# Kernel tuning notes

Hardware: AMD Instinct MI355X
Metric: run time of the kernel (lower is better)

## Reference

```python
import jax, jax.numpy as jnp
import numpy as np

NUM_REC = 22
P = 24            # nodes per graph
G = 8192          # graphs in batch
N = G * P         # 196608 nodes
E = N * 4         # 786432 edges (avg degree 4)
F_NODE = 96       # 74 chem features + 22 receptor one-hot
F_EDGE = 16
EPS = 1e-5
NEG_SLOPE = 0.2   # GATv2 default negative_slope


def gatv2(x, src, dst, edge_attr, Wl, bl, Wr, br, We, att, bo):
    """PyG GATv2Conv (heads=1, add_self_loops=True, fill_value='mean'), eval mode."""
    n = x.shape[0]
    # self loops with edge_attr = mean of incoming edge attrs per target node
    deg = jax.ops.segment_sum(jnp.ones_like(dst, dtype=x.dtype), dst, num_segments=n)
    loop_attr = jax.ops.segment_sum(edge_attr, dst, num_segments=n) / jnp.maximum(deg, 1.0)[:, None]
    loop = jnp.arange(n, dtype=src.dtype)
    s = jnp.concatenate([src, loop])           # [E+N] source
    d = jnp.concatenate([dst, loop])           # [E+N] target
    ea = jnp.concatenate([edge_attr, loop_attr], axis=0)
    xl = x @ Wl + bl                           # source transform [n, C]
    xr = x @ Wr + br                           # target transform [n, C]
    m = xl[s] + xr[d] + ea @ We                # [E+N, C]
    e = jax.nn.leaky_relu(m, NEG_SLOPE) @ att  # [E+N] attention logits
    # segment softmax over target nodes (every node has its self loop -> no empty segment)
    emax = jax.ops.segment_max(e, d, num_segments=n)
    ez = jnp.exp(e - emax[d])
    denom = jax.ops.segment_sum(ez, d, num_segments=n)
    alpha = ez / denom[d]
    return jax.ops.segment_sum(alpha[:, None] * xl[s], d, num_segments=n) + bo


def batchnorm(h, gamma, beta):
    # training-style BN (batch statistics, biased var) as in torch BatchNorm1d forward
    mu = h.mean(0)
    var = h.var(0)
    return gamma * (h - mu) * jax.lax.rsqrt(var + EPS) + beta


def setup_inputs() -> dict:
    key = jax.random.key(0)
    ks = jax.random.split(key, 40)
    x = jax.random.normal(ks[0], (N, F_NODE), jnp.float32)
    # intra-graph, self-loop-free edges
    src = jax.random.randint(ks[1], (E,), 0, N)
    off = jax.random.randint(ks[2], (E,), 1, P)
    dst = (src // P) * P + (src % P + off) % P
    edge_index = jnp.stack([src, dst]).astype(jnp.int32)
    edge_attr = jax.random.normal(ks[3], (E, F_EDGE), jnp.float32)
    batch = (jnp.arange(N) // P).astype(jnp.int32)

    def lin(k, i, o):
        return jax.random.normal(k, (i, o), jnp.float32) * 0.1

    def vec(k, o):
        return jax.random.normal(k, (o,), jnp.float32) * 0.1

    Fin = F_NODE - NUM_REC  # 74
    return {
        "x": x, "edge_index": edge_index, "edge_attr": edge_attr, "batch": batch,
        # GATv2 layer 1 (74 -> 32)
        "Wl1": lin(ks[4], Fin, 32), "bl1": vec(ks[5], 32),
        "Wr1": lin(ks[6], Fin, 32), "br1": vec(ks[7], 32),
        "We1": lin(ks[8], F_EDGE, 32), "att1": vec(ks[9], 32), "bo1": vec(ks[10], 32),
        # GATv2 layer 2 (32 -> 8)
        "Wl2": lin(ks[11], 32, 8), "bl2": vec(ks[12], 8),
        "Wr2": lin(ks[13], 32, 8), "br2": vec(ks[14], 8),
        "We2": lin(ks[15], F_EDGE, 8), "att2": vec(ks[16], 8), "bo2": vec(ks[17], 8),
        # BatchNorm affine
        "g1": jnp.ones((32,), jnp.float32), "be1": jnp.zeros((32,), jnp.float32),
        "g2": jnp.ones((8,), jnp.float32), "be2": jnp.zeros((8,), jnp.float32),
        # MLP head (8+22=30 -> 32 -> 16 -> 8 -> 4 -> 2)
        "fc1_W": lin(ks[18], 8 + NUM_REC, 32), "fc1_b": vec(ks[19], 32),
        "fc2_W": lin(ks[20], 32, 16), "fc2_b": vec(ks[21], 16),
        "fc3_W": lin(ks[22], 16, 8), "fc3_b": vec(ks[23], 8),
        "fc4_W": lin(ks[24], 8, 4), "fc4_b": vec(ks[25], 4),
        "out_W": lin(ks[26], 4, 2), "out_b": vec(ks[27], 2),
    }


def reference(x, edge_index, edge_attr, batch,
              Wl1, bl1, Wr1, br1, We1, att1, bo1,
              Wl2, bl2, Wr2, br2, We2, att2, bo2,
              g1, be1, g2, be2,
              fc1_W, fc1_b, fc2_W, fc2_b, fc3_W, fc3_b, fc4_W, fc4_b, out_W, out_b):
    src, dst = edge_index[0], edge_index[1]
    # per-graph receptor features = last NUM_REC cols of the first node of each graph
    first_idx = jnp.searchsorted(batch, jnp.arange(G, dtype=batch.dtype))
    rec_feat = x[first_idx, -NUM_REC:]                       # [G, 22]
    xin = x[:, :-NUM_REC]                                    # [N, 74]

    h = jax.nn.relu(gatv2(xin, src, dst, edge_attr, Wl1, bl1, Wr1, br1, We1, att1, bo1))
    h = batchnorm(h, g1, be1)                                # [N, 32]
    h = jax.nn.sigmoid(gatv2(h, src, dst, edge_attr, Wl2, bl2, Wr2, br2, We2, att2, bo2))
    h = batchnorm(h, g2, be2)                                # [N, 8]

    cnt = jax.ops.segment_sum(jnp.ones((x.shape[0], 1), x.dtype), batch, num_segments=G)
    pooled = jax.ops.segment_sum(h, batch, num_segments=G) / cnt  # global_mean_pool [G, 8]

    z = jnp.concatenate([pooled, rec_feat], axis=1)          # [G, 30]
    z = jax.nn.relu(z @ fc1_W + fc1_b)
    z = jax.nn.relu(z @ fc2_W + fc2_b)
    z = jax.nn.relu(z @ fc3_W + fc3_b)
    z = jax.nn.relu(z @ fc4_W + fc4_b)
    return z @ out_W + out_b                                 # [G, 2]
```

## Files before the change

kernel.cpp:

```cpp
#include <hip/hip_runtime.h>

typedef unsigned short u16;
typedef unsigned int   u32;
typedef __attribute__((ext_vector_type(4))) float f4_t;
typedef __attribute__((ext_vector_type(4))) unsigned short us4_t;

#define GG 8192
#define PP 24
#define NN 196608
#define EE 786432
#define CAP 176

#define oWl1 0
#define oWr1 2368
#define obl1 4736
#define obr1 4768
#define oWe1 4800
#define oatt1 5312
#define obo1 5344
#define oWl2 5376
#define oWr2 5632
#define obl2 5888
#define obr2 5896
#define oWe2 5904
#define oatt2 6032
#define obo2 6040
#define ofc1W 6048
#define ofc1b 7008
#define ofc2W 7040
#define ofc2b 7552
#define ofc3W 7568
#define ofc3b 7696
#define ofc4W 7704
#define ofc4b 7736
#define ooutW 7740
#define ooutb 7748

#define oW1I 0
#define oW2P 4864
#define oB2P 5376

__device__ __forceinline__ float bf2f(u16 u){
  union { u32 i; float f; } x; x.i = ((u32)u) << 16; return x.f;
}
__device__ __forceinline__ u32 fkey(float f){
  int i = __float_as_int(f);
  return (i >= 0) ? (((u32)i) | 0x80000000u) : ~((u32)i);
}
__device__ __forceinline__ float funkey(u32 k){
  u32 i = (k & 0x80000000u) ? (k & 0x7FFFFFFFu) : ~k;
  return __uint_as_float(i);
}
__device__ __forceinline__ float lrelu(float m){ return m > 0.f ? m : 0.2f*m; }
__device__ __forceinline__ float sexp(float a){ return __expf(fminf(a, 0.f)); }
__device__ __forceinline__ float ldf(const void* p, size_t i, int isf){
  return isf ? ((const float*)p)[i] : bf2f(((const u16*)p)[i]);
}

__global__ void k_zero(float* __restrict__ out){
  int i = blockIdx.x*256 + threadIdx.x;
  if(i < GG*2) out[i] = 0.f;
}

__global__ void k_count(const int* __restrict__ dst, int* __restrict__ cnt){
  int e = blockIdx.x*256 + threadIdx.x;
  if(e < EE){
    u32 d = (u32)dst[e];
    if(d < (u32)NN) atomicAdd(&cnt[d], 1);
  }
}

__global__ void k_scanA(const int* __restrict__ cnt, int* __restrict__ offs,
                        int* __restrict__ bsum){
  __shared__ int part[1024];
  int t = threadIdx.x;
  int i = blockIdx.x*1024 + t;
  int c = cnt[i];
  part[t] = c; __syncthreads();
  for(int off=1; off<1024; off<<=1){
    int v = (t>=off) ? part[t-off] : 0;
    __syncthreads();
    part[t] += v;
    __syncthreads();
  }
  offs[i] = part[t] - c;
  if(t==1023) bsum[blockIdx.x] = part[1023];
}

__global__ void k_scanB(int* __restrict__ bsum, int* __restrict__ offs){
  __shared__ int part[256];
  int t = threadIdx.x;
  int c = (t < 192) ? bsum[t] : 0;
  part[t] = c; __syncthreads();
  for(int off=1; off<256; off<<=1){
    int v = (t>=off) ? part[t-off] : 0;
    __syncthreads();
    part[t] += v;
    __syncthreads();
  }
  if(t < 192) bsum[t] = part[t] - c;
  if(t == 255) offs[NN] = part[255];
}

__global__ void k_scanC(int* __restrict__ offs, const int* __restrict__ bsum,
                        int* __restrict__ cursor){
  int t = threadIdx.x;
  int i = blockIdx.x*1024 + t;
  int v = offs[i] + bsum[blockIdx.x];
  offs[i] = v;
  cursor[i] = v;
}

__global__ void k_scatter(const int* __restrict__ src, const int* __restrict__ dst,
                          int* __restrict__ cursor, int* __restrict__ spack){
  int e = blockIdx.x*256 + threadIdx.x;
  if(e < EE){
    u32 d = (u32)dst[e];
    if(d >= (u32)NN) return;
    int g = d / PP;
    int pos = atomicAdd(&cursor[d], 1);
    if((u32)pos < (u32)EE){
      int sl = src[e] - g*PP;
      if((u32)sl > 23u) sl = 0;
      spack[pos] = sl | ((int)(d - g*PP) << 5) | (e << 10);
    }
  }
}

__global__ void k_eaperm(const int* __restrict__ spack, const int* __restrict__ offs,
                         const void* __restrict__ ea, const int* __restrict__ dflag,
                         float* __restrict__ eap){
  int i = blockIdx.x*256 + threadIdx.x;
  if(i >= EE) return;
  if(i >= offs[NN]) return;
  int isf = dflag[0];
  u32 id = ((u32)spack[i]) >> 10;
  if(id >= (u32)EE) id = 0;
  float* o = eap + (size_t)i*16;
  if(isf){
    const float* er = (const float*)ea + (size_t)id*16;
    #pragma unroll
    for(int q=0;q<4;q++) *(f4_t*)(o + q*4) = *(const f4_t*)(er + q*4);
  } else {
    const u16* er = (const u16*)ea + (size_t)id*16;
    #pragma unroll
    for(int c=0;c<16;c++) o[c] = bf2f(er[c]);
  }
}

__global__ void k_eapermB(const int* __restrict__ spack, const int* __restrict__ offs,
                          const void* __restrict__ ea, const int* __restrict__ dflag,
                          const float* __restrict__ wb,
                          float* __restrict__ eap, float* __restrict__ p2){
  int i = blockIdx.x*256 + threadIdx.x;
  if(i >= EE) return;
  if(i >= offs[NN]) return;
  int isf = dflag[0];
  u32 id = ((u32)spack[i]) >> 10;
  if(id >= (u32)EE) id = 0;
  float eav[16];
  if(isf){
    const float* er = (const float*)ea + (size_t)id*16;
    #pragma unroll
    for(int k=0;k<16;k++) eav[k] = er[k];
  } else {
    const u16* er = (const u16*)ea + (size_t)id*16;
    #pragma unroll
    for(int k=0;k<16;k++) eav[k] = bf2f(er[k]);
  }
  float* o = eap + (size_t)i*16;
  #pragma unroll
  for(int q=0;q<4;q++){
    f4_t r; r[0]=eav[q*4+0]; r[1]=eav[q*4+1]; r[2]=eav[q*4+2]; r[3]=eav[q*4+3];
    *(f4_t*)(o + q*4) = r;
  }
  float* o2 = p2 + (size_t)i*8;
  #pragma unroll
  for(int c=0;c<8;c+=4){
    float s0=0.f, s1=0.f, s2=0.f, s3=0.f;
    #pragma unroll
    for(int k=0;k<16;k++){
      f4_t w = *(const f4_t*)(wb + oWe2 + k*8 + c);
      s0 += eav[k]*w[0]; s1 += eav[k]*w[1]; s2 += eav[k]*w[2]; s3 += eav[k]*w[3];
    }
    f4_t r; r[0]=s0; r[1]=s1; r[2]=s2; r[3]=s3;
    *(f4_t*)(o2 + c) = r;
  }
}

__global__ void k_wconv(float* __restrict__ wb, float* __restrict__ wq, int* __restrict__ dflag,
    const u32* __restrict__ xw,
    const void* Wl1, const void* bl1, const void* Wr1, const void* br1,
    const void* We1, const void* att1, const void* bo1,
    const void* Wl2, const void* bl2, const void* Wr2, const void* br2,
    const void* We2, const void* att2, const void* bo2,
    const void* f1W, const void* f1b, const void* f2W, const void* f2b,
    const void* f3W, const void* f3b, const void* f4W, const void* f4b,
    const void* oW,  const void* ob)
{
  __shared__ u32 mx[256];
  int t = threadIdx.x;
  u32 m = 0;
  for(int i=t; i<2048; i+=256){
    u32 e = (xw[i] >> 7) & 0xFFu;
    m = m > e ? m : e;
  }
  mx[t] = m; __syncthreads();
  for(int off=128; off>0; off>>=1){
    if(t<off) mx[t] = mx[t] > mx[t+off] ? mx[t] : mx[t+off];
    __syncthreads();
  }
  int isf = (mx[0] > 140u) ? 1 : 0;
  if(t==0) dflag[0] = isf;
  #define CP(off,src,len) for(int i=t;i<(len);i+=256) wb[(off)+i]=ldf(src,i,isf);
  CP(oWl1,Wl1,2368) CP(oWr1,Wr1,2368) CP(obl1,bl1,32) CP(obr1,br1,32)
  CP(oWe1,We1,512)  CP(oatt1,att1,32) CP(obo1,bo1,32)
  CP(oWl2,Wl2,256)  CP(oWr2,Wr2,256)  CP(obl2,bl2,8)  CP(obr2,br2,8)
  CP(oWe2,We2,128)  CP(oatt2,att2,8)  CP(obo2,bo2,8)
  CP(ofc1W,f1W,960) CP(ofc1b,f1b,32)  CP(ofc2W,f2W,512) CP(ofc2b,f2b,16)
  CP(ofc3W,f3W,128) CP(ofc3b,f3b,8)   CP(ofc4W,f4W,32)  CP(ofc4b,f4b,4)
  CP(ooutW,oW,8)    CP(ooutb,ob,2)
  #undef CP
  for(int i=t; i<76*64; i+=256){
    int k = i>>6, cc = i&63, mat = cc>>5, c = cc&31;
    wq[oW1I + i] = (k < 74) ? ldf(mat ? Wr1 : Wl1, k*32 + c, isf) : 0.f;
  }
}

__global__ void k_prep2(float* __restrict__ wq, const float* __restrict__ wb,
                        const float* __restrict__ stats1){
  int t = threadIdx.x;
  for(int i=t; i<512; i+=256){
    int k = i>>4, cc = i&15, mat = cc>>3, c = cc&7;
    wq[oW2P + i] = stats1[k] * wb[(mat ? oWr2 : oWl2) + k*8 + c];
  }
  if(t < 16){
    int mat = t>>3, c = t&7;
    float s = wb[(mat ? obr2 : obl2) + c];
    for(int k=0;k<32;k++) s += stats1[32+k] * wb[(mat ? oWr2 : oWl2) + k*8 + c];
    wq[oB2P + t] = s;
  }
}

__global__ __launch_bounds__(256, 4) void k_l1stats_p(
    const void* __restrict__ x, const float* __restrict__ eap,
    const float* __restrict__ wb, const float* __restrict__ wq,
    const int* __restrict__ offs, const int* __restrict__ spack, const int* __restrict__ dflag,
    float* __restrict__ p1sum, float* __restrict__ p1sq,
    float* __restrict__ h1)
{
  __shared__ __align__(16) float sP[CAP][36];
  __shared__ __align__(16) float sXl[24][36];
  __shared__ __align__(16) float sXr[24][36];
  __shared__ __align__(16) float sPS[24][32];
  __shared__ __align__(16) float sPQ[24][32];
  __shared__ float sEv[CAP];
  __shared__ int   sSl[CAP];
  __shared__ int   sRO[25];

  const int t = threadIdx.x;
  const int g = blockIdx.x;
  const int isf = dflag[0];
  const int nb = g*PP;
  const int eb = offs[nb];
  int ecnt = offs[nb+24] - eb;
  if(ecnt < 0) ecnt = 0; if(ecnt > CAP) ecnt = CAP;

  if(t < 25){
    int v = offs[nb+t] - eb;
    if(v < 0) v = 0; if(v > CAP) v = CAP;
    sRO[t] = v;
  }
  for(int i=t; i<ecnt; i+=256){
    int sl = spack[eb+i] & 31; if(sl > 23) sl = 0;
    sSl[i] = sl;
  }

  {
    const int c = t & 31, mat = (t>>5)&1, w = t>>6, cc = t&63;
    const float* gW = wq + oW1I;
    float bi = wb[(mat ? obr1 : obl1) + c];
    float acc[6];
    #pragma unroll
    for(int j=0;j<6;j++) acc[j] = bi;
    if(isf){
      const float* xr0 = (const float*)x + (size_t)(nb + w*6)*96;
      for(int kb=0; kb<19; kb++){
        float w0 = gW[(kb*4+0)*64 + cc];
        float w1 = gW[(kb*4+1)*64 + cc];
        float w2 = gW[(kb*4+2)*64 + cc];
        float w3 = gW[(kb*4+3)*64 + cc];
        #pragma unroll
        for(int j=0;j<6;j++){
          f4_t xv = *(const f4_t*)(xr0 + (size_t)j*96 + kb*4);
          acc[j] += xv[0]*w0 + xv[1]*w1 + xv[2]*w2 + xv[3]*w3;
        }
      }
    } else {
      const u16* xr0 = (const u16*)x + (size_t)(nb + w*6)*96;
      for(int kb=0; kb<19; kb++){
        float w0 = gW[(kb*4+0)*64 + cc];
        float w1 = gW[(kb*4+1)*64 + cc];
        float w2 = gW[(kb*4+2)*64 + cc];
        float w3 = gW[(kb*4+3)*64 + cc];
        #pragma unroll
        for(int j=0;j<6;j++){
          us4_t xv = *(const us4_t*)(xr0 + (size_t)j*96 + kb*4);
          acc[j] += bf2f(xv[0])*w0 + bf2f(xv[1])*w1 + bf2f(xv[2])*w2 + bf2f(xv[3])*w3;
        }
      }
    }
    if(mat){
      #pragma unroll
      for(int j=0;j<6;j++) sXr[w*6+j][c] = acc[j];
    } else {
      #pragma unroll
      for(int j=0;j<6;j++) sXl[w*6+j][c] = acc[j];
    }
  }

  for(int i=t; i<ecnt*8; i+=256){
    int e = i>>3, q = i&7;
    const float* er = eap + (size_t)(eb+e)*16;
    float s0=0.f, s1=0.f, s2=0.f, s3=0.f;
    #pragma unroll
    for(int k=0;k<16;k++){
      float ev = er[k];
      f4_t w = *(const f4_t*)(wb + oWe1 + k*32 + q*4);
      s0 += ev*w[0]; s1 += ev*w[1]; s2 += ev*w[2]; s3 += ev*w[3];
    }
    f4_t r; r[0]=s0; r[1]=s1; r[2]=s2; r[3]=s3;
    *(f4_t*)&sP[e][q*4] = r;
  }
  __syncthreads();

  if(t < 192){
    const int r = t >> 3, sub = t & 7;
    const int a = sRO[r], b = sRO[r+1];
    const int deg = b - a;
    const float* att = wb + oatt1;

    float emax = -3.4e38f;
    for(int e=a+sub; e<b; e+=8){
      int sl = sSl[e];
      float ev = 0.f;
      #pragma unroll
      for(int q=0;q<8;q++){
        f4_t pv  = *(const f4_t*)&sP[e][q*4];
        f4_t xlv = *(const f4_t*)&sXl[sl][q*4];
        f4_t xrv = *(const f4_t*)&sXr[r][q*4];
        ev += att[q*4+0]*lrelu(xlv[0]+xrv[0]+pv[0]);
        ev += att[q*4+1]*lrelu(xlv[1]+xrv[1]+pv[1]);
        ev += att[q*4+2]*lrelu(xlv[2]+xrv[2]+pv[2]);
        ev += att[q*4+3]*lrelu(xlv[3]+xrv[3]+pv[3]);
      }
      sEv[e] = ev;
      emax = fmaxf(emax, ev);
    }
    emax = fmaxf(emax, __shfl_xor(emax, 1));
    emax = fmaxf(emax, __shfl_xor(emax, 2));
    emax = fmaxf(emax, __shfl_xor(emax, 4));

    float m0=0.f, m1=0.f, m2=0.f, m3=0.f;
    for(int e=a; e<b; ++e){
      f4_t pv = *(const f4_t*)&sP[e][sub*4];
      m0 += pv[0]; m1 += pv[1]; m2 += pv[2]; m3 += pv[3];
    }
    float invd = 1.f / (float)(deg > 0 ? deg : 1);
    float sv;
    {
      int c0 = sub*4;
      sv  = att[c0+0]*lrelu(sXl[r][c0+0] + sXr[r][c0+0] + m0*invd);
      sv += att[c0+1]*lrelu(sXl[r][c0+1] + sXr[r][c0+1] + m1*invd);
      sv += att[c0+2]*lrelu(sXl[r][c0+2] + sXr[r][c0+2] + m2*invd);
      sv += att[c0+3]*lrelu(sXl[r][c0+3] + sXr[r][c0+3] + m3*invd);
    }
    sv += __shfl_xor(sv, 1);
    sv += __shfl_xor(sv, 2);
    sv += __shfl_xor(sv, 4);

    float m = fmaxf(emax, sv);
    float ssum = 0.f;
    for(int e=a+sub; e<b; e+=8){
      float z = sexp(sEv[e] - m);
      sEv[e] = z;
      ssum += z;
    }
    ssum += __shfl_xor(ssum, 1);
    ssum += __shfl_xor(ssum, 2);
    ssum += __shfl_xor(ssum, 4);
    float selfZ = sexp(sv - m);
    float rden = 1.f / fmaxf(ssum + selfZ, 1e-30f);

    float a0=0.f, a1=0.f, a2=0.f, a3=0.f;
    for(int e=a; e<b; ++e){
      float z = sEv[e];
      f4_t xlv = *(const f4_t*)&sXl[sSl[e]][sub*4];
      a0 += z*xlv[0]; a1 += z*xlv[1]; a2 += z*xlv[2]; a3 += z*xlv[3];
    }
    f4_t xself = *(const f4_t*)&sXl[r][sub*4];
    f4_t outv, sqv;
    {
      float o;
      o = (a0 + selfZ*xself[0]) * rden; o = fmaxf(o + wb[obo1+sub*4+0], 0.f); outv[0]=o; sqv[0]=o*o;
      o = (a1 + selfZ*xself[1]) * rden; o = fmaxf(o + wb[obo1+sub*4+1], 0.f); outv[1]=o; sqv[1]=o*o;
      o = (a2 + selfZ*xself[2]) * rden; o = fmaxf(o + wb[obo1+sub*4+2], 0.f); outv[2]=o; sqv[2]=o*o;
      o = (a3 + selfZ*xself[3]) * rden; o = fmaxf(o + wb[obo1+sub*4+3], 0.f); outv[3]=o; sqv[3]=o*o;
    }
    *(f4_t*)&h1[((size_t)nb + r)*32 + sub*4] = outv;
    *(f4_t*)&sPS[r][sub*4] = outv;
    *(f4_t*)&sPQ[r][sub*4] = sqv;
  }
  __syncthreads();
  if(t < 32){
    float s=0.f, q=0.f;
    #pragma unroll
    for(int r=0;r<24;r++){ s += sPS[r][t]; q += sPQ[r][t]; }
    p1sum[g*32+t] = s; p1sq[g*32+t] = q;
  }
}

__global__ __launch_bounds__(256, 6) void k_fused2_p(
    const float* __restrict__ p2,
    const float* __restrict__ wb, const float* __restrict__ wq,
    const float* __restrict__ h1,
    const int* __restrict__ offs, const int* __restrict__ spack,
    float* __restrict__ gsum2, float* __restrict__ gsq2)
{
  __shared__ float sXl2[24][13];
  __shared__ float sXr2[24][13];
  __shared__ float sEv[CAP];
  __shared__ int   sSl[CAP];
  __shared__ int   sRO[25];
  __shared__ float sGS[24][8];
  __shared__ float sGQ[24][8];

  const int t = threadIdx.x;
  const int g = blockIdx.x;
  const int wid = t >> 6;
  const int lane = t & 63;
  const int nb = g*PP;
  const int eb = offs[nb];
  int ecnt = offs[nb+24] - eb;
  if(ecnt < 0) ecnt = 0; if(ecnt > CAP) ecnt = CAP;

  if(t < 25){
    int v = offs[nb+t] - eb;
    if(v < 0) v = 0; if(v > CAP) v = CAP;
    sRO[t] = v;
  }
  for(int i=t; i<ecnt; i+=256){
    int sl = spack[eb+i] & 31; if(sl > 23) sl = 0;
    sSl[i] = sl;
  }
  {
    int rz = wid*6;
    for(int i=lane; i<96; i+=64){
      int rl = i>>4, cc = i&15;
      int r = rz + rl;
      float s = wq[oB2P + cc];
      const float* hr = h1 + ((size_t)nb + r)*32;
      #pragma unroll
      for(int q=0;q<8;q++){
        f4_t hv = *(const f4_t*)(hr + q*4);
        s += hv[0]*wq[oW2P+(q*4+0)*16+cc] + hv[1]*wq[oW2P+(q*4+1)*16+cc]
           + hv[2]*wq[oW2P+(q*4+2)*16+cc] + hv[3]*wq[oW2P+(q*4+3)*16+cc];
      }
      if(cc < 8) sXl2[r][cc] = s; else sXr2[r][cc-8] = s;
    }
  }
  __syncthreads();

  if(t < 192){
    const int r = t >> 3, sub = t & 7;
    const int a = sRO[r], b = sRO[r+1];
    const int deg = b - a;
    const float* att2 = wb + oatt2;

    float emax = -3.4e38f;
    for(int e=a+sub; e<b; e+=8){
      int sl = sSl[e];
      const float* pe = p2 + (size_t)(eb+e)*8;
      float ev = 0.f;
      #pragma unroll
      for(int j=0;j<8;j++)
        ev += att2[j]*lrelu(sXl2[sl][j] + sXr2[r][j] + pe[j]);
      sEv[e] = ev;
      emax = fmaxf(emax, ev);
    }
    emax = fmaxf(emax, __shfl_xor(emax, 1));
    emax = fmaxf(emax, __shfl_xor(emax, 2));
    emax = fmaxf(emax, __shfl_xor(emax, 4));

    float mpc = 0.f;
    for(int e=a; e<b; ++e)
      mpc += p2[(size_t)(eb+e)*8 + sub];
    float invd = 1.f / (float)(deg > 0 ? deg : 1);
    float sv = att2[sub]*lrelu(sXl2[r][sub] + sXr2[r][sub] + mpc*invd);
    sv += __shfl_xor(sv, 1);
    sv += __shfl_xor(sv, 2);
    sv += __shfl_xor(sv, 4);

    float m = fmaxf(emax, sv);
    float ssum = 0.f;
    for(int e=a+sub; e<b; e+=8){
      float z = sexp(sEv[e] - m);
      sEv[e] = z;
      ssum += z;
    }
    ssum += __shfl_xor(ssum, 1);
    ssum += __shfl_xor(ssum, 2);
    ssum += __shfl_xor(ssum, 4);
    float selfZ = sexp(sv - m);
    float rden = 1.f / fmaxf(ssum + selfZ, 1e-30f);

    float acc = 0.f;
    for(int e=a; e<b; ++e)
      acc += sEv[e] * sXl2[sSl[e]][sub];
    float o = (acc + selfZ*sXl2[r][sub]) * rden;
    float s = 1.f / (1.f + __expf(-(o + wb[obo2+sub])));
    sGS[r][sub] = s;
    sGQ[r][sub] = s*s;
  }
  __syncthreads();
  if(t < 8){
    float gs=0.f, gq=0.f;
    #pragma unroll
    for(int r=0;r<24;r++){ gs += sGS[r][t]; gq += sGQ[r][t]; }
    gsum2[g*8+t] = gs; gsq2[g*8+t] = gq;
  }
}

__global__ __launch_bounds__(256, 6) void k_l1stats(
    const void* __restrict__ x, const void* __restrict__ ea, const float* __restrict__ eap,
    const float* __restrict__ wb, const float* __restrict__ wq,
    const int* __restrict__ offs, const int* __restrict__ spack, const int* __restrict__ dflag,
    float* __restrict__ p1sum, float* __restrict__ p1sq,
    float* __restrict__ h1, int use_h1)
{
  __shared__ __align__(16) float sEaF[CAP][16];
  __shared__ __align__(16) float sXl[24][36];
  __shared__ float sXr[24][33];
  __shared__ float sEaSum[24][17];
  __shared__ float sEv[CAP];
  __shared__ int   sSl[CAP];
  __shared__ int   sRO[25];
  __shared__ float sSelfE[24];
  __shared__ float sPS[4][32], sPQ[4][32];

  const int t = threadIdx.x;
  const int g = blockIdx.x;
  const int wid = t >> 6;
  const int lane = t & 63;
  const int isf = dflag[0];
  const int nb = g*PP;
  const int eb = offs[nb];
  int ecnt = offs[nb+24] - eb; if(ecnt < 0) ecnt = 0; if(ecnt > CAP) ecnt = CAP;

  if(t < 25){
    int v = offs[nb+t] - eb;
    if(v < 0) v = 0; if(v > CAP) v = CAP;
    sRO[t] = v;
  }
  if(eap){
    for(int i=t; i<ecnt; i+=256) sSl[i] = spack[eb+i] & 1023;
    for(int i=t; i<ecnt*4; i+=256){
      int e = i>>2, q = i&3;
      *(f4_t*)&sEaF[e][q*4] = *(const f4_t*)(eap + ((size_t)(eb+e))*16 + q*4);
    }
  } else {
    for(int i=t; i<ecnt; i+=256){
      int sp = spack[eb+i];
      sSl[i] = sp & 1023;
      u32 id = ((u32)sp) >> 10;
      if(id >= (u32)EE) id = 0;
      if(isf){
        const float* er = (const float*)ea + (size_t)id*16;
        #pragma unroll
        for(int q=0;q<4;q++) *(f4_t*)&sEaF[i][q*4] = *(const f4_t*)(er + q*4);
      } else {
        #pragma unroll
        for(int c=0;c<16;c++) sEaF[i][c] = bf2f(((const u16*)ea)[(size_t)id*16 + c]);
      }
    }
  }
  {
    int rz = wid*6;
    for(int i=lane; i<6*17; i+=64) sEaSum[rz + i/17][i%17] = 0.f;
  }

  {
    const int c = t & 31, mat = (t>>5)&1, w = wid, cc = t&63;
    const float* gW = wq + oW1I;
    float bi = wb[(mat ? obr1 : obl1) + c];
    float acc[6];
    #pragma unroll
    for(int j=0;j<6;j++) acc[j] = bi;
    if(isf){
      const float* xr0 = (const float*)x + (size_t)(nb + w*6)*96;
      for(int kb=0; kb<19; kb++){
        float w0 = gW[(kb*4+0)*64 + cc];
        float w1 = gW[(kb*4+1)*64 + cc];
        float w2 = gW[(kb*4+2)*64 + cc];
        float w3 = gW[(kb*4+3)*64 + cc];
        #pragma unroll
        for(int j=0;j<6;j++){
          f4_t xv = *(const f4_t*)(xr0 + (size_t)j*96 + kb*4);
          acc[j] += xv[0]*w0 + xv[1]*w1 + xv[2]*w2 + xv[3]*w3;
        }
      }
    } else {
      const u16* xr0 = (const u16*)x + (size_t)(nb + w*6)*96;
      for(int kb=0; kb<19; kb++){
        float w0 = gW[(kb*4+0)*64 + cc];
        float w1 = gW[(kb*4+1)*64 + cc];
        float w2 = gW[(kb*4+2)*64 + cc];
        float w3 = gW[(kb*4+3)*64 + cc];
        #pragma unroll
        for(int j=0;j<6;j++){
          us4_t xv = *(const us4_t*)(xr0 + (size_t)j*96 + kb*4);
          acc[j] += bf2f(xv[0])*w0 + bf2f(xv[1])*w1 + bf2f(xv[2])*w2 + bf2f(xv[3])*w3;
        }
      }
    }
    if(mat){
      #pragma unroll
      for(int j=0;j<6;j++) sXr[w*6+j][c] = acc[j];
    } else {
      #pragma unroll
      for(int j=0;j<6;j++) sXl[w*6+j][c] = acc[j];
    }
  }
  __syncthreads();

  const int r0 = wid*6;
  const int a0 = sRO[r0], a1 = sRO[r0+6];
  const int c = t & 31, eo = (t>>5)&1;

  float wr[16];
  #pragma unroll
  for(int k=0;k<16;k++) wr[k] = wb[oWe1 + k*32 + c];
  const float av = wb[oatt1 + c];
  const float bv = wb[obo1 + c];

  for(int base=a0; base<a1; base+=2){
    int e = base + eo;
    bool valid = (e < a1);
    int ec = valid ? e : a0;
    int sp = sSl[ec];
    int sl = sp & 31; if(sl > 23) sl = 0;
    int dl = (sp >> 5) & 31; if(dl > 23) dl = 0;
    f4_t A0 = *(const f4_t*)&sEaF[ec][0];
    f4_t A1 = *(const f4_t*)&sEaF[ec][4];
    f4_t A2 = *(const f4_t*)&sEaF[ec][8];
    f4_t A3 = *(const f4_t*)&sEaF[ec][12];
    float p = A0[0]*wr[0]+A0[1]*wr[1]+A0[2]*wr[2]+A0[3]*wr[3]
            + A1[0]*wr[4]+A1[1]*wr[5]+A1[2]*wr[6]+A1[3]*wr[7]
            + A2[0]*wr[8]+A2[1]*wr[9]+A2[2]*wr[10]+A2[3]*wr[11]
            + A3[0]*wr[12]+A3[1]*wr[13]+A3[2]*wr[14]+A3[3]*wr[15];
    if(valid && c < 16) atomicAdd(&sEaSum[dl][c], sEaF[ec][c]);
    float v = lrelu(sXl[sl][c] + sXr[dl][c] + p) * av;
    v += __shfl_xor(v, 16);
    v += __shfl_xor(v, 8);
    v += __shfl_xor(v, 4);
    v += __shfl_xor(v, 2);
    v += __shfl_xor(v, 1);
    if(valid && c == 0) sEv[e] = v;
  }

  #pragma unroll
  for(int rp=0; rp<3; rp++){
    int r = r0 + rp*2 + eo;
    int deg = sRO[r+1] - sRO[r];
    float invd = 1.f / (float)(deg > 0 ? deg : 1);
    float mp = 0.f;
    #pragma unroll
    for(int k=0;k<16;k++) mp += sEaSum[r][k] * wr[k];
    float v = lrelu(sXl[r][c] + sXr[r][c] + mp*invd) * av;
    v += __shfl_xor(v, 16);
    v += __shfl_xor(v, 8);
    v += __shfl_xor(v, 4);
    v += __shfl_xor(v, 2);
    v += __shfl_xor(v, 1);
    if(c == 0) sSelfE[r] = v;
  }

  float ps = 0.f, pq = 0.f;
  const int h = (t >> 5) & 1;
  #pragma unroll
  for(int j=0;j<6;j++){
    int r = r0 + j;
    int a = sRO[r], b = sRO[r+1];
    float selfE = sSelfE[r];
    float mx = -3.4e38f;
    for(int e=a+lane; e<b; e+=64) mx = fmaxf(mx, sEv[e]);
    mx = fmaxf(mx, __shfl_xor(mx, 32));
    mx = fmaxf(mx, __shfl_xor(mx, 16));
    mx = fmaxf(mx, __shfl_xor(mx, 8));
    mx = fmaxf(mx, __shfl_xor(mx, 4));
    mx = fmaxf(mx, __shfl_xor(mx, 2));
    mx = fmaxf(mx, __shfl_xor(mx, 1));
    float m = fmaxf(mx, selfE);
    float ds = 0.f;
    for(int e=a+lane; e<b; e+=64){
      float z = sexp(sEv[e] - m);
      sEv[e] = z;
      ds += z;
    }
    ds += __shfl_xor(ds, 32);
    ds += __shfl_xor(ds, 16);
    ds += __shfl_xor(ds, 8);
    ds += __shfl_xor(ds, 4);
    ds += __shfl_xor(ds, 2);
    ds += __shfl_xor(ds, 1);
// ... 193 lines not shown
    ds += __shfl_xor(ds, 8);
    ds += __shfl_xor(ds, 4);
    ds += __shfl_xor(ds, 2);
    ds += __shfl_xor(ds, 1);
    float selfZ = sexp(selfE - m);
    float rden = 1.f / fmaxf(ds + selfZ, 1e-30f);
    float acc = 0.f;
    for(int e=a+eo; e<b; e+=8){
      int sl = sSl[e] & 31; if(sl > 23) sl = 0;
      acc += sEv[e] * sXl2[sl][c];
    }
    acc += __shfl_xor(acc, 8);
    acc += __shfl_xor(acc, 16);
    acc += __shfl_xor(acc, 32);
    float out = (acc + selfZ * sXl2[r][c]) * rden;
    float s = 1.f / (1.f + __expf(-(out + bv)));
    if(eo == 0){ gs += s; gq += s*s; }
  }
  if(eo == 0){ sGS[wid][c] = gs; sGQ[wid][c] = gq; }
  __syncthreads();
  if(t < 8){
    gsum2[g*8+t] = sGS[0][t]+sGS[1][t]+sGS[2][t]+sGS[3][t];
    gsq2[g*8+t]  = sGQ[0][t]+sGQ[1][t]+sGQ[2][t]+sGQ[3][t];
  }
}

__global__ __launch_bounds__(256) void k_fused2_rec(
    const void* __restrict__ x, const void* __restrict__ ea,
    const float* __restrict__ wb, const float* __restrict__ stats1,
    const int* __restrict__ offs, const int* __restrict__ spack, const int* __restrict__ dflag,
    float* __restrict__ gsum2, float* __restrict__ gsq2)
{
  __shared__ float sXrow[24][76];
  __shared__ float sEaF[CAP][17];
  __shared__ __align__(16) float sXl[24][36];
  __shared__ __align__(16) float sXr[24][36];
  __shared__ __align__(16) float sOut[24][36];
  __shared__ float sH[24][33];
  __shared__ float sXl2[24][12], sXr2[24][12], sOut2[24][12];
  __shared__ float sEapSum[24][32];
  __shared__ float sEv[CAP], sEz[CAP];
  __shared__ int   sSp[CAP];
  __shared__ int   sDeg[24];
  __shared__ u32   sMaxU[24];
  __shared__ float sMaxF[24], sDen[24], sSelfZ[24];
  __shared__ float sAtt[32], sBo[32], sSc[32], sSh[32];

  const int t = threadIdx.x;
  const int g = blockIdx.x;
  const int isf = dflag[0];
  int eb = offs[g*24], ee = offs[(g+1)*24];
  if(eb < 0) eb = 0; if(eb > EE) eb = EE;
  if(ee < eb) ee = eb; if(ee > EE) ee = EE;
  int ecnt = ee - eb; if(ecnt > CAP) ecnt = CAP;

  for(int i=t; i<24*74; i+=256){
    int r = i/74, c = i%74;
    sXrow[r][c] = ldf(x, (size_t)(g*PP + r)*96 + c, isf);
  }
  for(int i=t; i<CAP; i+=256) sSp[i] = (i<ecnt) ? spack[eb+i] : 0;
  if(t < 32){ sAtt[t]=wb[oatt1+t]; sBo[t]=wb[obo1+t]; sSc[t]=stats1[t]; sSh[t]=stats1[32+t]; }
  if(t < 24){ sDeg[t]=0; sMaxU[t]=0u; sDen[t]=0.f; }
  for(int i=t; i<24*32; i+=256) sEapSum[i>>5][i&31] = 0.f;
  __syncthreads();
  for(int i=t; i<CAP*16; i+=256){
    int e = i>>4, c = i&15;
    float v = 0.f;
    if(e < ecnt){
      u32 id = ((u32)sSp[e]) >> 10;
      if(id >= (u32)EE) id = 0;
      v = ldf(ea, (size_t)id*16 + c, isf);
    }
    sEaF[e][c] = v;
  }
  __syncthreads();

  {
    int c = t & 31, rr0 = t >> 5;
    for(int r = rr0; r < 24; r += 8){
      float al = wb[obl1+c], ar = wb[obr1+c];
      for(int k=0;k<74;k++){
        float xv = sXrow[r][k];
        al += xv * wb[oWl1 + k*32 + c];
        ar += xv * wb[oWr1 + k*32 + c];
      }
      sXl[r][c] = al; sXr[r][c] = ar;
    }
  }
  __syncthreads();

  for(int e=t; e<ecnt; e+=256){
    int sp = sSp[e];
    int sl = sp & 31; if(sl > 23) sl = 0;
    int dl = (sp >> 5) & 31; if(dl > 23) dl = 0;
    float ev = 0.f;
    for(int c=0;c<32;c++){
      float p = 0.f;
      for(int k=0;k<16;k++) p += sEaF[e][k] * wb[oWe1 + k*32 + c];
      atomicAdd(&sEapSum[dl][c], p);
      ev += lrelu(sXl[sl][c] + sXr[dl][c] + p) * sAtt[c];
    }
    sEv[e] = ev;
    atomicMax(&sMaxU[dl], fkey(ev));
    atomicAdd(&sDeg[dl], 1);
  }
  __syncthreads();

  if(t < 24){
    float invd = 1.f / (float)(sDeg[t] > 0 ? sDeg[t] : 1);
    float ev = 0.f;
    for(int c=0;c<32;c++)
      ev += lrelu(sXl[t][c] + sXr[t][c] + sEapSum[t][c]*invd) * sAtt[c];
    float mxv = (sDeg[t] > 0) ? fmaxf(funkey(sMaxU[t]), ev) : ev;
    sMaxF[t] = mxv;
    float z = sexp(ev - mxv);
    sSelfZ[t] = z;
    sDen[t] = z;
  }
  __syncthreads();

  for(int e=t; e<ecnt; e+=256){
    int dl = (sSp[e]>>5)&31; if(dl > 23) dl = 0;
    float z = sexp(sEv[e] - sMaxF[dl]);
    sEz[e] = z;
    atomicAdd(&sDen[dl], z);
  }
  __syncthreads();

  for(int e=t; e<ecnt; e+=256){
    int dl = (sSp[e]>>5)&31; if(dl > 23) dl = 0;
    sEz[e] /= fmaxf(sDen[dl], 1e-30f);
  }
  if(t < 24) sSelfZ[t] /= fmaxf(sDen[t], 1e-30f);
  __syncthreads();

  for(int o=t; o<24*8; o+=256){
    int nl = o >> 3, cq = (o & 7)*4;
    float al = sSelfZ[nl];
    f4_t xv = *(const f4_t*)&sXl[nl][cq];
    f4_t r;
    #pragma unroll
    for(int j=0;j<4;j++) r[j] = al*xv[j];
    *(f4_t*)&sOut[nl][cq] = r;
  }
  __syncthreads();

  for(int o=t; o<ecnt*8; o+=256){
    int e = o >> 3, cq = (o & 7)*4;
    int sp = sSp[e];
    int sl = sp & 31; if(sl > 23) sl = 0;
    int dl = (sp >> 5) & 31; if(dl > 23) dl = 0;
    float al = sEz[e];
    f4_t xv = *(const f4_t*)&sXl[sl][cq];
    atomicAdd(&sOut[dl][cq+0], al*xv[0]);
    atomicAdd(&sOut[dl][cq+1], al*xv[1]);
    atomicAdd(&sOut[dl][cq+2], al*xv[2]);
    atomicAdd(&sOut[dl][cq+3], al*xv[3]);
  }
  __syncthreads();

  for(int i=t; i<24*32; i+=256){
    int r = i>>5, c = i&31;
    float v = fmaxf(sOut[r][c] + sBo[c], 0.f);
    sH[r][c] = v*sSc[c] + sSh[c];
  }
  __syncthreads();
  if(t < 24){ sDeg[t]=0; sMaxU[t]=0u; sDen[t]=0.f; }
  for(int i=t; i<24*8; i+=256) sEapSum[i>>3][i&7] = 0.f;
  __syncthreads();

  if(t < 24*8*2){
    int mat = t/192, rem = t%192, r = rem/8, c = rem&7;
    const float* Wm = wb + (mat ? oWr2 : oWl2);
    float s = wb[(mat ? obr2 : obl2) + c];
    for(int k=0;k<32;k++) s += sH[r][k]*Wm[k*8+c];
    if(mat) sXr2[r][c] = s; else sXl2[r][c] = s;
  }
  __syncthreads();

  for(int e=t; e<ecnt; e+=256){
    int sp = sSp[e];
    int sl = sp & 31; if(sl > 23) sl = 0;
    int dl = (sp >> 5) & 31; if(dl > 23) dl = 0;
    float ev = 0.f;
    for(int c=0;c<8;c++){
      float p = 0.f;
      for(int k=0;k<16;k++) p += sEaF[e][k] * wb[oWe2 + k*8 + c];
      atomicAdd(&sEapSum[dl][c], p);
      ev += lrelu(sXl2[sl][c] + sXr2[dl][c] + p) * wb[oatt2+c];
    }
    sEv[e] = ev;
    atomicMax(&sMaxU[dl], fkey(ev));
    atomicAdd(&sDeg[dl], 1);
  }
  __syncthreads();

  if(t < 24){
    float invd = 1.f / (float)(sDeg[t] > 0 ? sDeg[t] : 1);
    float ev = 0.f;
    for(int c=0;c<8;c++)
      ev += lrelu(sXl2[t][c] + sXr2[t][c] + sEapSum[t][c]*invd) * wb[oatt2+c];
    float mxv = (sDeg[t] > 0) ? fmaxf(funkey(sMaxU[t]), ev) : ev;
    sMaxF[t] = mxv;
    float z = sexp(ev - mxv);
    sSelfZ[t] = z;
    sDen[t] = z;
  }
  __syncthreads();

  for(int e=t; e<ecnt; e+=256){
    int dl = (sSp[e]>>5)&31; if(dl > 23) dl = 0;
    float z = sexp(sEv[e] - sMaxF[dl]);
    sEz[e] = z;
    atomicAdd(&sDen[dl], z);
  }
  __syncthreads();

  for(int e=t; e<ecnt; e+=256){
    int dl = (sSp[e]>>5)&31; if(dl > 23) dl = 0;
    sEz[e] /= fmaxf(sDen[dl], 1e-30f);
  }
  if(t < 24) sSelfZ[t] /= fmaxf(sDen[t], 1e-30f);
  __syncthreads();

  for(int o=t; o<24*8; o+=256){
    int nl = o >> 3, c = o & 7;
    sOut2[nl][c] = sSelfZ[nl] * sXl2[nl][c];
  }
  __syncthreads();

  for(int o=t; o<ecnt*8; o+=256){
    int e = o >> 3, c = o & 7;
    int sp = sSp[e];
    int sl = sp & 31; if(sl > 23) sl = 0;
    int dl = (sp >> 5) & 31; if(dl > 23) dl = 0;
    atomicAdd(&sOut2[dl][c], sEz[e]*sXl2[sl][c]);
  }
  __syncthreads();

  if(t < 8){
    float gs=0.f, gq=0.f;
    for(int nl=0; nl<24; nl++){
      float v = sOut2[nl][t] + wb[obo2+t];
      float s = 1.f / (1.f + __expf(-v));
      gs += s; gq += s*s;
    }
    gsum2[g*8+t] = gs; gsq2[g*8+t] = gq;
  }
}

__global__ __launch_bounds__(256) void k_mlp(
    const float* __restrict__ gsum2, const float* __restrict__ stats2,
    const void* __restrict__ x, const int* __restrict__ dflag,
    const float* __restrict__ wb, float* __restrict__ out)
{
  __shared__ float w[1702];
  int t = threadIdx.x;
  for(int i=t; i<1702; i+=256) w[i] = wb[6048+i];
  __syncthreads();
  int g = blockIdx.x*256 + t;
  int isf = dflag[0];
  float a[30], b[32];
  for(int c=0;c<8;c++) a[c] = stats2[c]*(gsum2[(size_t)g*8+c]*(1.f/24.f)) + stats2[8+c];
  size_t xoff = (size_t)g*PP*96 + 74;
  for(int j=0;j<22;j++) a[8+j] = ldf(x, xoff+j, isf);
  for(int o=0;o<32;o++){ float s = w[960+o];  for(int i=0;i<30;i++) s += a[i]*w[i*32+o];      b[o]=fmaxf(s,0.f); }
  for(int o=0;o<16;o++){ float s = w[1504+o]; for(int i=0;i<32;i++) s += b[i]*w[992+i*16+o];  a[o]=fmaxf(s,0.f); }
  for(int o=0;o<8;o++){  float s = w[1648+o]; for(int i=0;i<16;i++) s += a[i]*w[1520+i*8+o];  b[o]=fmaxf(s,0.f); }
  for(int o=0;o<4;o++){  float s = w[1688+o]; for(int i=0;i<8;i++)  s += b[i]*w[1656+i*4+o];  a[o]=fmaxf(s,0.f); }
  for(int o=0;o<2;o++){
    float s = w[1700+o];
    for(int i=0;i<4;i++) s += a[i]*w[1692+i*2+o];
    out[(size_t)g*2+o] = s;
  }
}

extern "C" void kernel_launch(void* const* d_in, const int* in_sizes, int n_in,
                              void* d_out, int out_size, void* d_ws, size_t ws_size,
                              hipStream_t stream)
{
  (void)in_sizes; (void)n_in; (void)out_size;
  const void* x    = d_in[0];
  const int* eidx  = (const int*)d_in[1];
  const void* ea   = d_in[2];

  const int* srcA = eidx;
  const int* dstA = eidx + EE;

  constexpr size_t O_WB    = 0;
  constexpr size_t O_WQ    = 32768;
  constexpr size_t O_OFFS  = 57344;
  constexpr size_t O_CUR   = O_OFFS + (size_t)(NN+512)*4;
  constexpr size_t O_SPACK = O_CUR  + (size_t)NN*4;
  constexpr size_t O_P1S   = O_SPACK + (size_t)EE*4;
  constexpr size_t O_P1Q   = O_P1S   + (size_t)GG*32*4;
  constexpr size_t O_ST1   = O_P1Q   + (size_t)GG*32*4;
  constexpr size_t O_GS2   = O_ST1   + 256;
  constexpr size_t O_GQ2   = O_GS2   + (size_t)GG*8*4;
  constexpr size_t O_ST2   = O_GQ2   + (size_t)GG*8*4;
  constexpr size_t O_FLAG  = O_ST2   + 256;
  constexpr size_t REQUIRED_BASE = O_FLAG + 256;
  constexpr size_t O_H1    = REQUIRED_BASE;
  constexpr size_t REQUIRED_BIG = O_H1 + (size_t)NN*32*4;
  constexpr size_t O_EAP1  = REQUIRED_BIG;
  constexpr size_t O_P2    = O_EAP1 + (size_t)EE*16*4;
  constexpr size_t REQUIRED_P = O_P2 + (size_t)EE*8*4;
  constexpr size_t REQUIRED_EAP16 = O_EAP1 + (size_t)EE*16*4;

  if(ws_size < REQUIRED_BASE){
    k_zero<<<(GG*2+255)/256, 256, 0, stream>>>((float*)d_out);
    return;
  }
  const int use_h1  = (ws_size >= REQUIRED_BIG)   ? 1 : 0;
  const int use_p   = (ws_size >= REQUIRED_P)     ? 1 : 0;
  const int use_eap = (!use_p && ws_size >= REQUIRED_EAP16) ? 1 : 0;

  char* W = (char*)d_ws;
  float* wb     = (float*)(W + O_WB);
  float* wq     = (float*)(W + O_WQ);
  int*   offs   = (int*)(W + O_OFFS);
  int*   bsum   = offs + NN + 64;
  int*   cnt    = (int*)(W + O_CUR);
  int*   cursor = (int*)(W + O_CUR);
  int*   spack  = (int*)(W + O_SPACK);
  float* p1sum  = (float*)(W + O_P1S);
  float* p1sq   = (float*)(W + O_P1Q);
  float* stats1 = (float*)(W + O_ST1);
  float* gsum2  = (float*)(W + O_GS2);
  float* gsq2   = (float*)(W + O_GQ2);
  float* stats2 = (float*)(W + O_ST2);
  int*   dflag  = (int*)(W + O_FLAG);
  float* h1     = (float*)(W + O_H1);
  float* eap1   = (float*)(W + O_EAP1);
  float* p2     = (float*)(W + O_P2);

  hipMemsetAsync(cnt, 0, (size_t)NN*sizeof(int), stream);
  k_count  <<<EE/256, 256, 0, stream>>>(dstA, cnt);
  k_scanA  <<<192, 1024, 0, stream>>>(cnt, offs, bsum);
  k_scanB  <<<1, 256, 0, stream>>>(bsum, offs);
  k_scanC  <<<192, 1024, 0, stream>>>(offs, bsum, cursor);
  k_scatter<<<EE/256, 256, 0, stream>>>(srcA, dstA, cursor, spack);
  k_wconv  <<<1, 256, 0, stream>>>(wb, wq, dflag, (const u32*)x,
            d_in[4], d_in[5], d_in[6], d_in[7], d_in[8], d_in[9], d_in[10],
            d_in[11], d_in[12], d_in[13], d_in[14], d_in[15], d_in[16], d_in[17],
            d_in[22], d_in[23], d_in[24], d_in[25], d_in[26], d_in[27],
            d_in[28], d_in[29], d_in[30], d_in[31]);
  if(use_p){
    k_eapermB<<<EE/256, 256, 0, stream>>>(spack, offs, ea, dflag, wb, eap1, p2);
    k_l1stats_p<<<GG, 256, 0, stream>>>(x, eap1, wb, wq, offs, spack, dflag,
                                        p1sum, p1sq, h1);
  } else {
    if(use_eap)
      k_eaperm<<<EE/256, 256, 0, stream>>>(spack, offs, ea, dflag, eap1);
    k_l1stats<<<GG, 256, 0, stream>>>(x, ea, use_eap ? eap1 : (float*)nullptr,
                                      wb, wq, offs, spack, dflag,
                                      p1sum, p1sq, h1, use_h1);
  }
  k_reduce <<<32, 256, 0, stream>>>(p1sum, p1sq, d_in[18], d_in[19], dflag, stats1, 32);
  k_prep2  <<<1, 256, 0, stream>>>(wq, wb, stats1);
  if(use_p)
    k_fused2_p<<<GG, 256, 0, stream>>>(p2, wb, wq, h1, offs, spack, gsum2, gsq2);
  else if(use_h1)
    k_fused2_h1<<<GG, 256, 0, stream>>>(ea, use_eap ? eap1 : (float*)nullptr,
                                        wb, wq, h1, offs, spack, dflag, gsum2, gsq2);
  else
    k_fused2_rec<<<GG, 256, 0, stream>>>(x, ea, wb, stats1, offs, spack, dflag, gsum2, gsq2);
  k_reduce <<<8, 256, 0, stream>>>(gsum2, gsq2, d_in[20], d_in[21], dflag, stats2, 8);
  k_mlp    <<<GG/256, 256, 0, stream>>>(gsum2, stats2, x, dflag, wb, (float*)d_out);
}
```

Before: 591.1 us.

## Fuse edge-attr permutation and layer-2 edge projection into layer-1 kernel

Removes the separate k_eapermB pass that wrote a permuted 16-float edge-attribute buffer. The layer-1 per-graph kernel now gathers edge attributes directly through the sorted edge ids and also computes and stores the layer-2 edge projection p2. It drops the pad on sP in favour of an XOR swizzle, reuses sP for the BN partial sums, and raises launch_bounds occupancy to 5 to fit the smaller shared footprint. The trade-off is uncoalesced gathers of edge rows, each read twice inside the kernel, in exchange for removing a large intermediate write and read plus one launch.

```diff
diff --git a/kernel.cpp b/kernel.cpp
--- a/kernel.cpp
+++ b/kernel.cpp
@@ -148,46 +148,6 @@
   }
 }
 
-__global__ void k_eapermB(const int* __restrict__ spack, const int* __restrict__ offs,
-                          const void* __restrict__ ea, const int* __restrict__ dflag,
-                          const float* __restrict__ wb,
-                          float* __restrict__ eap, float* __restrict__ p2){
-  int i = blockIdx.x*256 + threadIdx.x;
-  if(i >= EE) return;
-  if(i >= offs[NN]) return;
-  int isf = dflag[0];
-  u32 id = ((u32)spack[i]) >> 10;
-  if(id >= (u32)EE) id = 0;
-  float eav[16];
-  if(isf){
-    const float* er = (const float*)ea + (size_t)id*16;
-    #pragma unroll
-    for(int k=0;k<16;k++) eav[k] = er[k];
-  } else {
-    const u16* er = (const u16*)ea + (size_t)id*16;
-    #pragma unroll
-    for(int k=0;k<16;k++) eav[k] = bf2f(er[k]);
-  }
-  float* o = eap + (size_t)i*16;
-  #pragma unroll
-  for(int q=0;q<4;q++){
-    f4_t r; r[0]=eav[q*4+0]; r[1]=eav[q*4+1]; r[2]=eav[q*4+2]; r[3]=eav[q*4+3];
-    *(f4_t*)(o + q*4) = r;
-  }
-  float* o2 = p2 + (size_t)i*8;
-  #pragma unroll
-  for(int c=0;c<8;c+=4){
-    float s0=0.f, s1=0.f, s2=0.f, s3=0.f;
-    #pragma unroll
-    for(int k=0;k<16;k++){
-      f4_t w = *(const f4_t*)(wb + oWe2 + k*8 + c);
-      s0 += eav[k]*w[0]; s1 += eav[k]*w[1]; s2 += eav[k]*w[2]; s3 += eav[k]*w[3];
-    }
-    f4_t r; r[0]=s0; r[1]=s1; r[2]=s2; r[3]=s3;
-    *(f4_t*)(o2 + c) = r;
-  }
-}
-
 __global__ void k_wconv(float* __restrict__ wb, float* __restrict__ wq, int* __restrict__ dflag,
     const u32* __restrict__ xw,
     const void* Wl1, const void* bl1, const void* Wr1, const void* br1,
@@ -242,18 +202,16 @@
   }
 }
 
-__global__ __launch_bounds__(256, 4) void k_l1stats_p(
-    const void* __restrict__ x, const float* __restrict__ eap,
+__global__ __launch_bounds__(256, 5) void k_l1stats_p(
+    const void* __restrict__ x, const void* __restrict__ ea,
     const float* __restrict__ wb, const float* __restrict__ wq,
     const int* __restrict__ offs, const int* __restrict__ spack, const int* __restrict__ dflag,
     float* __restrict__ p1sum, float* __restrict__ p1sq,
-    float* __restrict__ h1)
+    float* __restrict__ h1, float* __restrict__ p2)
 {
-  __shared__ __align__(16) float sP[CAP][36];
+  __shared__ __align__(16) float sP[CAP][32];
   __shared__ __align__(16) float sXl[24][36];
   __shared__ __align__(16) float sXr[24][36];
-  __shared__ __align__(16) float sPS[24][32];
-  __shared__ __align__(16) float sPQ[24][32];
   __shared__ float sEv[CAP];
   __shared__ int   sSl[CAP];
   __shared__ int   sRO[25];
@@ -321,21 +279,58 @@
 
   for(int i=t; i<ecnt*8; i+=256){
     int e = i>>3, q = i&7;
-    const float* er = eap + (size_t)(eb+e)*16;
+    u32 id = ((u32)spack[eb+e]) >> 10;
+    if(id >= (u32)EE) id = 0;
+    float ev[16];
+    if(isf){
+      const float* er = (const float*)ea + (size_t)id*16;
+      #pragma unroll
+      for(int k=0;k<16;k++) ev[k] = er[k];
+    } else {
+      const u16* er = (const u16*)ea + (size_t)id*16;
+      #pragma unroll
+      for(int k=0;k<16;k++) ev[k] = bf2f(er[k]);
+    }
     float s0=0.f, s1=0.f, s2=0.f, s3=0.f;
     #pragma unroll
     for(int k=0;k<16;k++){
-      float ev = er[k];
       f4_t w = *(const f4_t*)(wb + oWe1 + k*32 + q*4);
-      s0 += ev*w[0]; s1 += ev*w[1]; s2 += ev*w[2]; s3 += ev*w[3];
+      s0 += ev[k]*w[0]; s1 += ev[k]*w[1]; s2 += ev[k]*w[2]; s3 += ev[k]*w[3];
     }
     f4_t r; r[0]=s0; r[1]=s1; r[2]=s2; r[3]=s3;
-    *(f4_t*)&sP[e][q*4] = r;
-  }
-  __syncthreads();
-
+    *(f4_t*)&sP[e][((q ^ (e&7))*4)] = r;
+  }
+
+  for(int i=t; i<ecnt*2; i+=256){
+    int e = i>>1, half = i&1;
+    u32 id = ((u32)spack[eb+e]) >> 10;
+    if(id >= (u32)EE) id = 0;
+    float ev[16];
+    if(isf){
+      const float* er = (const float*)ea + (size_t)id*16;
+      #pragma unroll
+      for(int k=0;k<16;k++) ev[k] = er[k];
+    } else {
+      const u16* er = (const u16*)ea + (size_t)id*16;
+      #pragma unroll
+      for(int k=0;k<16;k++) ev[k] = bf2f(er[k]);
+    }
+    float s0=0.f, s1=0.f, s2=0.f, s3=0.f;
+    #pragma unroll
+    for(int k=0;k<16;k++){
+      f4_t w = *(const f4_t*)(wb + oWe2 + k*8 + half*4);
+      s0 += ev[k]*w[0]; s1 += ev[k]*w[1]; s2 += ev[k]*w[2]; s3 += ev[k]*w[3];
+    }
+    f4_t r; r[0]=s0; r[1]=s1; r[2]=s2; r[3]=s3;
+    *(f4_t*)(p2 + (size_t)(eb+e)*8 + half*4) = r;
+  }
+  __syncthreads();
+
+  f4_t outv = {0.f,0.f,0.f,0.f}, sqv = {0.f,0.f,0.f,0.f};
+  int rr = 0, ss = 0;
   if(t < 192){
     const int r = t >> 3, sub = t & 7;
+    rr = r; ss = sub;
     const int a = sRO[r], b = sRO[r+1];
     const int deg = b - a;
     const float* att = wb + oatt1;
@@ -343,10 +338,11 @@
     float emax = -3.4e38f;
     for(int e=a+sub; e<b; e+=8){
       int sl = sSl[e];
+      int ex = e & 7;
       float ev = 0.f;
       #pragma unroll
       for(int q=0;q<8;q++){
-        f4_t pv  = *(const f4_t*)&sP[e][q*4];
+        f4_t pv  = *(const f4_t*)&sP[e][((q ^ ex)*4)];
         f4_t xlv = *(const f4_t*)&sXl[sl][q*4];
         f4_t xrv = *(const f4_t*)&sXr[r][q*4];
         ev += att[q*4+0]*lrelu(xlv[0]+xrv[0]+pv[0]);
@@ -363,7 +359,7 @@
 
     float m0=0.f, m1=0.f, m2=0.f, m3=0.f;
     for(int e=a; e<b; ++e){
-      f4_t pv = *(const f4_t*)&sP[e][sub*4];
+      f4_t pv = *(const f4_t*)&sP[e][((sub ^ (e&7))*4)];
       m0 += pv[0]; m1 += pv[1]; m2 += pv[2]; m3 += pv[3];
     }
     float invd = 1.f / (float)(deg > 0 ? deg : 1);
@@ -399,7 +395,6 @@
       a0 += z*xlv[0]; a1 += z*xlv[1]; a2 += z*xlv[2]; a3 += z*xlv[3];
     }
     f4_t xself = *(const f4_t*)&sXl[r][sub*4];
-    f4_t outv, sqv;
     {
       float o;
       o = (a0 + selfZ*xself[0]) * rden; o = fmaxf(o + wb[obo1+sub*4+0], 0.f); outv[0]=o; sqv[0]=o*o;
@@ -408,8 +403,14 @@
       o = (a3 + selfZ*xself[3]) * rden; o = fmaxf(o + wb[obo1+sub*4+3], 0.f); outv[3]=o; sqv[3]=o*o;
     }
     *(f4_t*)&h1[((size_t)nb + r)*32 + sub*4] = outv;
-    *(f4_t*)&sPS[r][sub*4] = outv;
-    *(f4_t*)&sPQ[r][sub*4] = sqv;
+  }
+  __syncthreads();
+
+  float (*sPS)[32] = (float(*)[32])&sP[0][0];
+  float (*sPQ)[32] = (float(*)[32])&sP[24][0];
+  if(t < 192){
+    *(f4_t*)&sPS[rr][ss*4] = outv;
+    *(f4_t*)&sPQ[rr][ss*4] = sqv;
   }
   __syncthreads();
   if(t < 32){
@@ -1209,17 +1210,16 @@
   constexpr size_t REQUIRED_BASE = O_FLAG + 256;
   constexpr size_t O_H1    = REQUIRED_BASE;
   constexpr size_t REQUIRED_BIG = O_H1 + (size_t)NN*32*4;
-  constexpr size_t O_EAP1  = REQUIRED_BIG;
-  constexpr size_t O_P2    = O_EAP1 + (size_t)EE*16*4;
-  constexpr size_t REQUIRED_P = O_P2 + (size_t)EE*8*4;
-  constexpr size_t REQUIRED_EAP16 = O_EAP1 + (size_t)EE*16*4;
+  constexpr size_t O_AUX   = REQUIRED_BIG;
+  constexpr size_t REQUIRED_P     = O_AUX + (size_t)EE*8*4;
+  constexpr size_t REQUIRED_EAP16 = O_AUX + (size_t)EE*16*4;
 
   if(ws_size < REQUIRED_BASE){
     k_zero<<<(GG*2+255)/256, 256, 0, stream>>>((float*)d_out);
     return;
   }
   const int use_h1  = (ws_size >= REQUIRED_BIG)   ? 1 : 0;
-  const int use_p   = (ws_size >= REQUIRED_P)     ? 1 : 0;
+  const int use_p   = (use_h1 && ws_size >= REQUIRED_P) ? 1 : 0;
   const int use_eap = (!use_p && ws_size >= REQUIRED_EAP16) ? 1 : 0;
 
   char* W = (char*)d_ws;
@@ -1238,8 +1238,7 @@
   float* stats2 = (float*)(W + O_ST2);
   int*   dflag  = (int*)(W + O_FLAG);
   float* h1     = (float*)(W + O_H1);
-  float* eap1   = (float*)(W + O_EAP1);
-  float* p2     = (float*)(W + O_P2);
+  float* aux    = (float*)(W + O_AUX);
 
   hipMemsetAsync(cnt, 0, (size_t)NN*sizeof(int), stream);
   k_count  <<<EE/256, 256, 0, stream>>>(dstA, cnt);
@@ -1253,22 +1252,21 @@
             d_in[22], d_in[23], d_in[24], d_in[25], d_in[26], d_in[27],
             d_in[28], d_in[29], d_in[30], d_in[31]);
   if(use_p){
-    k_eapermB<<<EE/256, 256, 0, stream>>>(spack, offs, ea, dflag, wb, eap1, p2);
-    k_l1stats_p<<<GG, 256, 0, stream>>>(x, eap1, wb, wq, offs, spack, dflag,
-                                        p1sum, p1sq, h1);
+    k_l1stats_p<<<GG, 256, 0, stream>>>(x, ea, wb, wq, offs, spack, dflag,
+                                        p1sum, p1sq, h1, aux);
   } else {
     if(use_eap)
-      k_eaperm<<<EE/256, 256, 0, stream>>>(spack, offs, ea, dflag, eap1);
-    k_l1stats<<<GG, 256, 0, stream>>>(x, ea, use_eap ? eap1 : (float*)nullptr,
+      k_eaperm<<<EE/256, 256, 0, stream>>>(spack, offs, ea, dflag, aux);
+    k_l1stats<<<GG, 256, 0, stream>>>(x, ea, use_eap ? aux : (float*)nullptr,
                                       wb, wq, offs, spack, dflag,
                                       p1sum, p1sq, h1, use_h1);
   }
   k_reduce <<<32, 256, 0, stream>>>(p1sum, p1sq, d_in[18], d_in[19], dflag, stats1, 32);
   k_prep2  <<<1, 256, 0, stream>>>(wq, wb, stats1);
   if(use_p)
-    k_fused2_p<<<GG, 256, 0, stream>>>(p2, wb, wq, h1, offs, spack, gsum2, gsq2);
+    k_fused2_p<<<GG, 256, 0, stream>>>(aux, wb, wq, h1, offs, spack, gsum2, gsq2);
   else if(use_h1)
-    k_fused2_h1<<<GG, 256, 0, stream>>>(ea, use_eap ? eap1 : (float*)nullptr,
+    k_fused2_h1<<<GG, 256, 0, stream>>>(ea, use_eap ? aux : (float*)nullptr,
                                         wb, wq, h1, offs, spack, dflag, gsum2, gsq2);
   else
     k_fused2_rec<<<GG, 256, 0, stream>>>(x, ea, wb, stats1, offs, spack, dflag, gsum2, gsq2);
```

Result: slower. 651.5 us (+10.2%).
